# Performance work log

Hardware: AMD Instinct MI355X
Metric: run time of the kernel (lower is better)

The kernel has to match this reference:

```python
import jax, jax.numpy as jnp
import numpy as np

N = 50000
E = 800000
NODE_IN = 64
EDGE_IN = 8
OUT = 1
SAGE_DIMS = [(64, 64), (64, 64), (64, 32), (32, 32)]
EDGE_DIMS = [(8, 64), (64, 64), (64, 32), (32, 32)]


def setup_inputs():
    key = jax.random.key(0)
    keys = iter(jax.random.split(key, 64))
    d = {}
    d["x"] = jax.random.normal(next(keys), (N, NODE_IN), jnp.float32)
    d["dis"] = jax.random.normal(next(keys), (E, EDGE_IN), jnp.float32)
    d["edge_index"] = jax.random.randint(next(keys), (2, E), 0, N, dtype=jnp.int32)
    for i, (fi, fo) in enumerate(SAGE_DIMS):
        d[f"s{i}_wl"] = jax.random.normal(next(keys), (fi, fo), jnp.float32) / np.sqrt(fi).astype(np.float32)
        d[f"s{i}_bl"] = jnp.zeros((fo,), jnp.float32)
        d[f"s{i}_wr"] = jax.random.normal(next(keys), (fi, fo), jnp.float32) / np.sqrt(fi).astype(np.float32)
    for i, (fi, h) in enumerate(EDGE_DIMS):
        d[f"e{i}_w1"] = jax.random.normal(next(keys), (fi, 2 * h), jnp.float32) / np.sqrt(fi).astype(np.float32)
        d[f"e{i}_b1"] = jnp.zeros((2 * h,), jnp.float32)
        d[f"e{i}_w2"] = jax.random.normal(next(keys), (2 * h, h), jnp.float32) / np.sqrt(2 * h).astype(np.float32)
        d[f"e{i}_b2"] = jnp.zeros((h,), jnp.float32)
    d["fc_w"] = jax.random.normal(next(keys), (64, OUT), jnp.float32) / 8.0
    d["fc_b"] = jnp.zeros((OUT,), jnp.float32)
    return d


def _sage(x, row, col, wl, bl, wr):
    # PyG SAGEConv (aggr='mean'): lin_l(mean_{j->i} x_j) + lin_r(x_i); lin_l has bias.
    msg = x[row]  # [E, F] gather of source features
    s = jax.ops.segment_sum(msg, col, num_segments=N)
    cnt = jax.ops.segment_sum(jnp.ones((row.shape[0], 1), x.dtype), col, num_segments=N)
    mean = s / jnp.maximum(cnt, 1.0)  # isolated nodes -> 0 (matches scatter-mean)
    return mean @ wl + bl + x @ wr


def _edge_conv(dis, col, w1, b1, w2, b2):
    # EdgeOnlyConv: add_self_loops with num_nodes=E and zero edge_attr, so the
    # output has E rows; self-loop message = lin(0) = b1 and each segment t gets
    # mean = (sum_{edges->t} lin(dis) + b1) / (deg_in(t) + 1); then lin_update.
    msg = dis @ w1 + b1  # [E, 2h]
    s = jax.ops.segment_sum(msg, col, num_segments=E)
    deg = jax.ops.segment_sum(jnp.ones((col.shape[0], 1), dis.dtype), col, num_segments=E)
    aggr = (s + b1) / (deg + 1.0)
    return aggr @ w2 + b2


def _forward(x, dis, edge_index, sage_params, edge_params, fc_w, fc_b):
    row, col = edge_index[0], edge_index[1]
    h = x
    for wl, bl, wr in sage_params:
        h = jax.nn.leaky_relu(_sage(h, row, col, wl, bl, wr))
    d = dis
    for w1, b1, w2, b2 in edge_params:
        d = jax.nn.leaky_relu(_edge_conv(d, col, w1, b1, w2, b2))
    # dropout is identity at inference
    feats = jnp.concatenate([h[row] * h[col], d], axis=1)  # [E, hidden]
    return feats @ fc_w + fc_b


def reference(x, dis, edge_index, s0_wl, s0_bl, s0_wr, s1_wl, s1_bl, s1_wr, s2_wl, s2_bl, s2_wr, s3_wl, s3_bl, s3_wr, e0_w1, e0_b1, e0_w2, e0_b2, e1_w1, e1_b1, e1_w2, e1_b2, e2_w1, e2_b1, e2_w2, e2_b2, e3_w1, e3_b1, e3_w2, e3_b2, fc_w, fc_b):
    sage_params = [(s0_wl, s0_bl, s0_wr), (s1_wl, s1_bl, s1_wr), (s2_wl, s2_bl, s2_wr), (s3_wl, s3_bl, s3_wr)]
    edge_params = [(e0_w1, e0_b1, e0_w2, e0_b2), (e1_w1, e1_b1, e1_w2, e1_b2), (e2_w1, e2_b1, e2_w2, e2_b2), (e3_w1, e3_b1, e3_w2, e3_b2)]
    return _forward(x, dis, edge_index, sage_params, edge_params, fc_w, fc_b)
```

## Files before the change

kernel.cpp:

```cpp
#include <hip/hip_runtime.h>

#define LRELU(v) ((v) > 0.0f ? (v) : 0.01f * (v))

__device__ __forceinline__ unsigned short f2bf(float f) {
    union { float f; unsigned u; } c;
    c.f = f;
    return (unsigned short)((c.u + 0x7fffu + ((c.u >> 16) & 1)) >> 16);
}
__device__ __forceinline__ float bf_lo(unsigned u) {
    union { unsigned i; float f; } v;
    v.i = u << 16;
    return v.f;
}
__device__ __forceinline__ float bf_hi(unsigned u) {
    union { unsigned i; float f; } v;
    v.i = u & 0xffff0000u;
    return v.f;
}

__global__ void bucket_count_k(const int* __restrict__ col, int* __restrict__ bcnt, int E) {
    __shared__ int lcnt[512];
    int tid = threadIdx.x;
    for (int i = tid; i < 512; i += 1024) lcnt[i] = 0;
    __syncthreads();
    int base = blockIdx.x * 8192;
    for (int k = 0; k < 8; ++k) {
        int e = base + k * 1024 + tid;
        if (e < E) atomicAdd(&lcnt[col[e] >> 7], 1);
    }
    __syncthreads();
    for (int i = tid; i < 512; i += 1024) {
        int v = lcnt[i];
        if (v) atomicAdd(&bcnt[i], v);
    }
}

__global__ void bucket_scan_k(const int* __restrict__ bcnt, int* __restrict__ bbase,
                              int* __restrict__ bwp, int NBUCK, int E) {
    __shared__ int s[512];
    int tid = threadIdx.x;
    int v = (tid < NBUCK) ? bcnt[tid] : 0;
    s[tid] = v;
    __syncthreads();
    for (int off = 1; off < 512; off <<= 1) {
        int t = (tid >= off) ? s[tid - off] : 0;
        __syncthreads();
        s[tid] += t;
        __syncthreads();
    }
    if (tid < NBUCK) {
        int ex = s[tid] - v;
        bbase[tid] = ex;
        bwp[tid] = ex;
    }
    if (tid == 0) bbase[NBUCK] = E;
}

__global__ void bucket_scatter_k(const int* __restrict__ row, const int* __restrict__ col,
                                 int* __restrict__ bwp, int2* __restrict__ tmp, int E) {
    __shared__ int lcnt[512];
    __shared__ int gbase[512];
    int tid = threadIdx.x;
    for (int i = tid; i < 512; i += 1024) lcnt[i] = 0;
    __syncthreads();
    int base = blockIdx.x * 8192;
    int lpos[8], bk[8];
    for (int k = 0; k < 8; ++k) {
        int e = base + k * 1024 + tid;
        if (e < E) {
            int b = col[e] >> 7;
            bk[k] = b;
            lpos[k] = atomicAdd(&lcnt[b], 1);
        } else
            bk[k] = -1;
    }
    __syncthreads();
    for (int i = tid; i < 512; i += 1024) {
        int v = lcnt[i];
        gbase[i] = v ? atomicAdd(&bwp[i], v) : 0;
    }
    __syncthreads();
    for (int k = 0; k < 8; ++k) {
        int e = base + k * 1024 + tid;
        if (e < E) {
            int c = col[e];
            tmp[gbase[bk[k]] + lpos[k]] = make_int2(row[e], ((c & 127) << 25) | e);
        }
    }
}

__global__ void bucket_csr_k(const int2* __restrict__ tmp, const int* __restrict__ bbase,
                             int* __restrict__ rowptr, int* __restrict__ cnt,
                             int2* __restrict__ pairs, int N, int E) {
    constexpr int CAP = 6144;
    __shared__ int2 buf[CAP];
    __shared__ int lcnt[128];
    __shared__ int sscan[128];
    __shared__ int lwp[128];
    int b = blockIdx.x;
    int tid = threadIdx.x;
    int s = bbase[b], e = bbase[b + 1];
    int sz = e - s;
    if (tid < 128) lcnt[tid] = 0;
    __syncthreads();
    for (int i = tid; i < sz; i += 256) {
        int2 v = tmp[s + i];
        if (i < CAP) buf[i] = v;
        atomicAdd(&lcnt[((unsigned)v.y) >> 25], 1);
    }
    __syncthreads();
    if (tid < 128) sscan[tid] = lcnt[tid];
    __syncthreads();
    for (int off = 1; off < 128; off <<= 1) {
        int t = (tid < 128 && tid >= off) ? sscan[tid - off] : 0;
        __syncthreads();
        if (tid < 128) sscan[tid] += t;
        __syncthreads();
    }
    if (tid < 128) {
        int ex = sscan[tid] - lcnt[tid];
        lwp[tid] = ex;
        int c = b * 128 + tid;
        if (c < N) {
            rowptr[c] = s + ex;
            cnt[c] = lcnt[tid];
            if (c == N - 1) rowptr[N] = E;
        }
    }
    __syncthreads();
    for (int i = tid; i < sz; i += 256) {
        int2 v = (i < CAP) ? buf[i] : tmp[s + i];
        int cl = ((unsigned)v.y) >> 25;
        int p = atomicAdd(&lwp[cl], 1);
        pairs[s + p] = make_int2(v.x, v.y & 0x1FFFFFF);
    }
}

template <int FIN, int FOUT, bool BFL>
__global__ void gemm2_k(const float* __restrict__ h, const float* __restrict__ wl,
                        const float* __restrict__ wr, const float* __restrict__ bl,
                        void* __restrict__ hl, float* __restrict__ hr, int N) {
    constexpr int XT = (2 * FOUT) / 4;
    constexpr int YT = 256 / XT;
    constexpr int NPT = 4;
    constexpr int NPB = YT * NPT;
    __shared__ float sw[FIN * 2 * FOUT];
    int lin = threadIdx.y * XT + threadIdx.x;
    for (int idx = lin; idx < FIN * FOUT; idx += 256) {
        int f = idx / FOUT, o = idx % FOUT;
        sw[f * 2 * FOUT + o] = wl[idx];
        sw[f * 2 * FOUT + FOUT + o] = wr[idx];
    }
    __syncthreads();
    int og = threadIdx.x * 4;
    int base = blockIdx.x * NPB + threadIdx.y * NPT;
    int ix[NPT] = {min(base + 0, N - 1), min(base + 1, N - 1), min(base + 2, N - 1),
                   min(base + 3, N - 1)};
    float4 s[NPT] = {{0.f, 0.f, 0.f, 0.f}, {0.f, 0.f, 0.f, 0.f}, {0.f, 0.f, 0.f, 0.f},
                     {0.f, 0.f, 0.f, 0.f}};
#pragma unroll 2
    for (int f = 0; f < FIN; f += 4) {
        float4 w0 = *(const float4*)&sw[(f + 0) * 2 * FOUT + og];
        float4 w1 = *(const float4*)&sw[(f + 1) * 2 * FOUT + og];
        float4 w2 = *(const float4*)&sw[(f + 2) * 2 * FOUT + og];
        float4 w3 = *(const float4*)&sw[(f + 3) * 2 * FOUT + og];
#pragma unroll
        for (int k = 0; k < NPT; ++k) {
            float4 v = *(const float4*)(h + (size_t)ix[k] * FIN + f);
            s[k].x += v.x * w0.x + v.y * w1.x + v.z * w2.x + v.w * w3.x;
            s[k].y += v.x * w0.y + v.y * w1.y + v.z * w2.y + v.w * w3.y;
            s[k].z += v.x * w0.z + v.y * w1.z + v.z * w2.z + v.w * w3.z;
            s[k].w += v.x * w0.w + v.y * w1.w + v.z * w2.w + v.w * w3.w;
        }
    }
    bool isR = og >= FOUT;
    int oo = isR ? og - FOUT : og;
    if (isR) {
        float4 bias = *(const float4*)&bl[oo];
#pragma unroll
        for (int k = 0; k < NPT; ++k) {
            int i = base + k;
            if (i < N) {
                float4 r = {s[k].x + bias.x, s[k].y + bias.y, s[k].z + bias.z, s[k].w + bias.w};
                *(float4*)(hr + (size_t)i * FOUT + oo) = r;
            }
        }
    } else {
#pragma unroll
        for (int k = 0; k < NPT; ++k) {
            int i = base + k;
            if (i < N) {
                if (BFL) {
                    unsigned short* d = (unsigned short*)hl + (size_t)i * FOUT + oo;
                    *(ushort4*)d =
                        make_ushort4(f2bf(s[k].x), f2bf(s[k].y), f2bf(s[k].z), f2bf(s[k].w));
                } else {
                    *(float4*)((float*)hl + (size_t)i * FOUT + oo) = s[k];
                }
            }
        }
    }
}

__global__ void aggr_fused64_bf_k(const unsigned short* __restrict__ hlb,
                                  const float* __restrict__ hr, const int* __restrict__ rowptr,
                                  const int2* __restrict__ pairs, float* __restrict__ out, int N) {
    int wave = (blockIdx.x * blockDim.x + threadIdx.x) >> 6;
    int lane = threadIdx.x & 63;
    if (wave >= N) return;
    int u = lane >> 4, f4 = lane & 15;
    int s = rowptr[wave], e = rowptr[wave + 1];
    float4 a = {0.f, 0.f, 0.f, 0.f};
    int p = s + u;
    for (; p + 4 < e; p += 8) {
        int r0 = pairs[p].x, r1 = pairs[p + 4].x;
        uint2 v0 = ((const uint2*)(hlb + (size_t)r0 * 64))[f4];
        uint2 v1 = ((const uint2*)(hlb + (size_t)r1 * 64))[f4];
        a.x += bf_lo(v0.x) + bf_lo(v1.x);
        a.y += bf_hi(v0.x) + bf_hi(v1.x);
        a.z += bf_lo(v0.y) + bf_lo(v1.y);
        a.w += bf_hi(v0.y) + bf_hi(v1.y);
    }
    if (p < e) {
        uint2 v = ((const uint2*)(hlb + (size_t)pairs[p].x * 64))[f4];
        a.x += bf_lo(v.x); a.y += bf_hi(v.x); a.z += bf_lo(v.y); a.w += bf_hi(v.y);
    }
    a.x += __shfl_down(a.x, 32); a.y += __shfl_down(a.y, 32);
    a.z += __shfl_down(a.z, 32); a.w += __shfl_down(a.w, 32);
    a.x += __shfl_down(a.x, 16); a.y += __shfl_down(a.y, 16);
    a.z += __shfl_down(a.z, 16); a.w += __shfl_down(a.w, 16);
    if (lane < 16) {
        float inv = 1.0f / fmaxf((float)(e - s), 1.0f);
        float4 r = ((const float4*)(hr + (size_t)wave * 64))[f4];
        float4 o;
        o.x = LRELU(a.x * inv + r.x);
        o.y = LRELU(a.y * inv + r.y);
        o.z = LRELU(a.z * inv + r.z);
        o.w = LRELU(a.w * inv + r.w);
        ((float4*)(out + (size_t)wave * 64))[f4] = o;
    }
}

template <bool OUTBF>
__global__ void aggr_fused32_bf_k(const unsigned short* __restrict__ hlb,
                                  const float* __restrict__ hr, const int* __restrict__ rowptr,
                                  const int2* __restrict__ pairs, void* __restrict__ out, int N) {
    int wave = (blockIdx.x * blockDim.x + threadIdx.x) >> 6;
    int lane = threadIdx.x & 63;
    if (wave >= N) return;
    int u = lane >> 3, f4 = lane & 7;
    int s = rowptr[wave], e = rowptr[wave + 1];
    float4 a = {0.f, 0.f, 0.f, 0.f};
    int p = s + u;
    for (; p + 8 < e; p += 16) {
        int r0 = pairs[p].x, r1 = pairs[p + 8].x;
        uint2 v0 = ((const uint2*)(hlb + (size_t)r0 * 32))[f4];
        uint2 v1 = ((const uint2*)(hlb + (size_t)r1 * 32))[f4];
        a.x += bf_lo(v0.x) + bf_lo(v1.x);
        a.y += bf_hi(v0.x) + bf_hi(v1.x);
        a.z += bf_lo(v0.y) + bf_lo(v1.y);
        a.w += bf_hi(v0.y) + bf_hi(v1.y);
    }
    if (p < e) {
        uint2 v = ((const uint2*)(hlb + (size_t)pairs[p].x * 32))[f4];
        a.x += bf_lo(v.x); a.y += bf_hi(v.x); a.z += bf_lo(v.y); a.w += bf_hi(v.y);
    }
    a.x += __shfl_down(a.x, 32); a.y += __shfl_down(a.y, 32);
    a.z += __shfl_down(a.z, 32); a.w += __shfl_down(a.w, 32);
    a.x += __shfl_down(a.x, 16); a.y += __shfl_down(a.y, 16);
    a.z += __shfl_down(a.z, 16); a.w += __shfl_down(a.w, 16);
    a.x += __shfl_down(a.x, 8); a.y += __shfl_down(a.y, 8);
    a.z += __shfl_down(a.z, 8); a.w += __shfl_down(a.w, 8);
    if (lane < 8) {
        float inv = 1.0f / fmaxf((float)(e - s), 1.0f);
        const float4* hp = (const float4*)(hr + (size_t)wave * 32);
        float4 r = hp[f4];
        float4 o;
        o.x = LRELU(a.x * inv + r.x);
        o.y = LRELU(a.y * inv + r.y);
        o.z = LRELU(a.z * inv + r.z);
        o.w = LRELU(a.w * inv + r.w);
        if (OUTBF) {
            unsigned short* d = (unsigned short*)out + (size_t)wave * 32 + f4 * 4;
            *(ushort4*)d = make_ushort4(f2bf(o.x), f2bf(o.y), f2bf(o.z), f2bf(o.w));
        } else {
            ((float4*)((float*)out + (size_t)wave * 32))[f4] = o;
        }
    }
}

__global__ void edge_aggr8_k(const float* __restrict__ dis, const int* __restrict__ rowptr,
                             const int2* __restrict__ pairs, float* __restrict__ sd, int N) {
    int wave = (blockIdx.x * blockDim.x + threadIdx.x) >> 6;
    int lane = threadIdx.x & 63;
    if (wave >= N) return;
    int u = lane >> 1, f4 = lane & 1;
    int s = rowptr[wave], e = rowptr[wave + 1];
    float4 a = {0.f, 0.f, 0.f, 0.f};
    for (int p = s + u; p < e; p += 32) {
        const float4* dp = (const float4*)(dis + (size_t)pairs[p].y * 8);
        float4 v = dp[f4];
        a.x += v.x; a.y += v.y; a.z += v.z; a.w += v.w;
    }
    for (int off = 32; off >= 2; off >>= 1) {
        a.x += __shfl_down(a.x, off); a.y += __shfl_down(a.y, off);
        a.z += __shfl_down(a.z, off); a.w += __shfl_down(a.w, off);
    }
    if (lane < 2) ((float4*)(sd + (size_t)wave * 8))[f4] = a;
}

template <int H2, int HOUT>
__device__ __forceinline__ void w12_body(const float* __restrict__ w1,
                                         const float* __restrict__ w2, float* __restrict__ out,
                                         int i, int o) {
    float s = 0.0f;
#pragma unroll
    for (int k = 0; k < H2; ++k) s += w1[i * H2 + k] * w2[k * HOUT + o];
    out[i * HOUT + o] = s;
}

__global__ void gemm_w12_all_k(const float* __restrict__ w1_0, const float* __restrict__ w2_0,
                               float* __restrict__ o0, const float* __restrict__ w1_1,
                               const float* __restrict__ w2_1, float* __restrict__ o1,
                               const float* __restrict__ w1_2, const float* __restrict__ w2_2,
                               float* __restrict__ o2, const float* __restrict__ w1_3,
                               const float* __restrict__ w2_3, float* __restrict__ o3) {
    int b = blockIdx.x;
    int o = threadIdx.x;
    if (b < 8) {
        w12_body<128, 64>(w1_0, w2_0, o0, b, o);
    } else if (b < 72) {
        w12_body<128, 64>(w1_1, w2_1, o1, b - 8, o);
    } else if (b < 136) {
        if (o < 32) w12_body<64, 32>(w1_2, w2_2, o2, b - 72, o);
    } else {
        if (o < 32) w12_body<64, 32>(w1_3, w2_3, o3, b - 136, o);
    }
}

template <int FIN, int FOUT>
__global__ void edge_compute_scatter_k(const float* __restrict__ sd, const int* __restrict__ cnt,
                                       const float* __restrict__ w12, const float* __restrict__ mw2,
                                       const float* __restrict__ b1w2, const float* __restrict__ b2,
                                       const float* __restrict__ cnext,
                                       const int* __restrict__ col, float* __restrict__ sdnext,
                                       int N) {
    constexpr int ROWS = 256 / FOUT;
    constexpr int NPT = 4;
    constexpr int NPB = ROWS * NPT;
    __shared__ float sw[FIN * FOUT];
    int lin = threadIdx.y * FOUT + threadIdx.x;
    for (int idx = lin; idx < FIN * FOUT; idx += 256) sw[idx] = w12[idx];
    __syncthreads();
    int o = threadIdx.x;
    int base = blockIdx.x * NPB + threadIdx.y * NPT;
    int ix[NPT] = {min(base + 0, N - 1), min(base + 1, N - 1), min(base + 2, N - 1),
                   min(base + 3, N - 1)};
    float s[NPT] = {0.f, 0.f, 0.f, 0.f};
#pragma unroll 2
    for (int f = 0; f < FIN; f += 4) {
        float w0 = sw[(f + 0) * FOUT + o], w1 = sw[(f + 1) * FOUT + o];
        float w2 = sw[(f + 2) * FOUT + o], w3 = sw[(f + 3) * FOUT + o];
#pragma unroll
        for (int k = 0; k < NPT; ++k) {
            float4 v = *(const float4*)(sd + (size_t)ix[k] * FIN + f);
            s[k] += v.x * w0 + v.y * w1 + v.z * w2 + v.w * w3;
        }
    }
    float mo = mw2[o], bo = b1w2[o], b2o = b2[o], co = cnext[o];
#pragma unroll
    for (int k = 0; k < NPT; ++k) {
        int i = base + k;
        if (i < N) {
            float deg = (float)cnt[i];
            float inv = 1.0f / (deg + 1.0f);
            float val = LRELU((s[k] + deg * mo + bo) * inv + b2o);
            atomicAdd(&sdnext[(size_t)col[i] * FOUT + o], val - co);
        }
    }
}

template <int FIN, int FOUT>
__global__ void edge_compute2_k(const float* __restrict__ sd, const int* __restrict__ cnt,
                                const float* __restrict__ w12, const float* __restrict__ mw2,
                                const float* __restrict__ b1w2, const float* __restrict__ b2,
                                float* __restrict__ out, int N) {
    constexpr int ROWS = 256 / FOUT;
    constexpr int NPT = 4;
    constexpr int NPB = ROWS * NPT;
    __shared__ float sw[FIN * FOUT];
    int lin = threadIdx.y * FOUT + threadIdx.x;
    for (int idx = lin; idx < FIN * FOUT; idx += 256) sw[idx] = w12[idx];
    __syncthreads();
    int o = threadIdx.x;
    int base = blockIdx.x * NPB + threadIdx.y * NPT;
    int ix[NPT] = {min(base + 0, N - 1), min(base + 1, N - 1), min(base + 2, N - 1),
                   min(base + 3, N - 1)};
    float s[NPT] = {0.f, 0.f, 0.f, 0.f};
#pragma unroll 2
    for (int f = 0; f < FIN; f += 4) {
        float w0 = sw[(f + 0) * FOUT + o], w1 = sw[(f + 1) * FOUT + o];
        float w2 = sw[(f + 2) * FOUT + o], w3 = sw[(f + 3) * FOUT + o];
#pragma unroll
        for (int k = 0; k < NPT; ++k) {
            float4 v = *(const float4*)(sd + (size_t)ix[k] * FIN + f);
            s[k] += v.x * w0 + v.y * w1 + v.z * w2 + v.w * w3;
        }
    }
    float mo = mw2[o], bo = b1w2[o], b2o = b2[o];
#pragma unroll
    for (int k = 0; k < NPT; ++k) {
        int i = base + k;
        if (i < N) {
            float deg = (float)cnt[i];
            float inv = 1.0f / (deg + 1.0f);
            out[(size_t)i * FOUT + o] = LRELU((s[k] + deg * mo + bo) * inv + b2o);
        }
    }
}

__global__ void consts_k(const float* __restrict__ e0_b1, const float* __restrict__ e0_w2,
                         const float* __restrict__ e0_b2, const float* __restrict__ e1_b1,
                         const float* __restrict__ e1_w2, const float* __restrict__ e1_b2,
                         const float* __restrict__ e2_b1, const float* __restrict__ e2_w2,
                         const float* __restrict__ e2_b2, const float* __restrict__ e3_b1,
                         const float* __restrict__ e3_w2, const float* __restrict__ e3_b2,
                         const float* __restrict__ w12_1, const float* __restrict__ w12_2,
                         const float* __restrict__ w12_3, float* __restrict__ cbuf) {
    __shared__ float c1[64], c2[64], c3[32];
    int tid = threadIdx.x;
    if (tid < 64) {
        float s = 0.0f;
#pragma unroll
        for (int k = 0; k < 128; ++k) s += e0_b1[k] * e0_w2[k * 64 + tid];
        cbuf[192 + tid] = s;
        c1[tid] = LRELU(s + e0_b2[tid]);
        cbuf[tid] = c1[tid];
    }
    if (tid < 64) {
        float s = 0.0f;
#pragma unroll
        for (int k = 0; k < 128; ++k) s += e1_b1[k] * e1_w2[k * 64 + tid];
        cbuf[256 + tid] = s;
        c2[tid] = LRELU(s + e1_b2[tid]);
        cbuf[64 + tid] = c2[tid];
    }
    if (tid < 32) {
        float s = 0.0f;
#pragma unroll
        for (int k = 0; k < 64; ++k) s += e2_b1[k] * e2_w2[k * 32 + tid];
        cbuf[384 + tid] = s;
        c3[tid] = LRELU(s + e2_b2[tid]);
        cbuf[128 + tid] = c3[tid];
    }
    if (tid < 32) {
        float s = 0.0f;
#pragma unroll
        for (int k = 0; k < 64; ++k) s += e3_b1[k] * e3_w2[k * 32 + tid];
        cbuf[448 + tid] = s;
        cbuf[160 + tid] = LRELU(s + e3_b2[tid]);
    }
    __syncthreads();
    if (tid < 64) {
        float s = cbuf[256 + tid];
#pragma unroll
        for (int f = 0; f < 64; ++f) s += c1[f] * w12_1[f * 64 + tid];
        cbuf[320 + tid] = s;
    }
    if (tid < 32) {
        float s = cbuf[384 + tid];
#pragma unroll
        for (int f = 0; f < 64; ++f) s += c2[f] * w12_2[f * 32 + tid];
        cbuf[416 + tid] = s;
    }
    if (tid < 32) {
        float s = cbuf[448 + tid];
#pragma unroll
        for (int f = 0; f < 32; ++f) s += c3[f] * w12_3[f * 32 + tid];
        cbuf[480 + tid] = s;
    }
}

__device__ __forceinline__ float bdot8(uint4 a, uint4 b, const float* __restrict__ w) {
    return bf_lo(a.x) * bf_lo(b.x) * w[0] + bf_hi(a.x) * bf_hi(b.x) * w[1] +
           bf_lo(a.y) * bf_lo(b.y) * w[2] + bf_hi(a.y) * bf_hi(b.y) * w[3] +
           bf_lo(a.z) * bf_lo(b.z) * w[4] + bf_hi(a.z) * bf_hi(b.z) * w[5] +
           bf_lo(a.w) * bf_lo(b.w) * w[6] + bf_hi(a.w) * bf_hi(b.w) * w[7];
}

__global__ void final_k(const unsigned short* __restrict__ h3b, const float* __restrict__ dv3,
                        const float* __restrict__ c4, const int* __restrict__ row,
                        const int* __restrict__ col, const float* __restrict__ fcw,
                        const float* __restrict__ fcb, float* __restrict__ out, int E, int N) {
    __shared__ float sw[64];
    __shared__ float sc4[32];
    __shared__ float cdot_s;
    int tid = threadIdx.x;
    if (tid < 64) sw[tid] = fcw[tid];
    if (tid < 32) sc4[tid] = c4[tid];
    __syncthreads();
    if (tid == 0) {
        float cd = 0.0f;
#pragma unroll
        for (int k = 0; k < 32; ++k) cd += sc4[k] * sw[32 + k];
        cdot_s = cd;
    }
    __syncthreads();
    float fb = fcb[0];
    float cdot = cdot_s;
    int e0 = blockIdx.x * 512 + tid;
    int e1 = e0 + 256;
    bool v0 = e0 < E, v1 = e1 < E;
    int r0 = 0, c0 = 0, r1 = 0, c1 = 0;
    if (v0) { r0 = row[e0]; c0 = col[e0]; }
    if (v1) { r1 = row[e1]; c1 = col[e1]; }
    uint4 a00, a01, b00, b01, a10, a11, b10, b11;
    if (v0) {
        const uint4* pr = (const uint4*)(h3b + (size_t)r0 * 32);
        const uint4* pc = (const uint4*)(h3b + (size_t)c0 * 32);
        a00 = pr[0]; a01 = pr[1]; b00 = pc[0]; b01 = pc[1];
    }
    if (v1) {
        const uint4* pr = (const uint4*)(h3b + (size_t)r1 * 32);
        const uint4* pc = (const uint4*)(h3b + (size_t)c1 * 32);
        a10 = pr[0]; a11 = pr[1]; b10 = pc[0]; b11 = pc[1];
    }
    if (v0) {
        float s = fb + bdot8(a00, b00, sw) + bdot8(a01, b01, sw + 8) +
                  bdot8(((const uint4*)(h3b + (size_t)r0 * 32))[2],
                        ((const uint4*)(h3b + (size_t)c0 * 32))[2], sw + 16) +
                  bdot8(((const uint4*)(h3b + (size_t)r0 * 32))[3],
                        ((const uint4*)(h3b + (size_t)c0 * 32))[3], sw + 24);
        if (e0 < N) {
            const float4* dp = (const float4*)(dv3 + (size_t)e0 * 32);
#pragma unroll
            for (int q = 0; q < 8; ++q) {
                float4 d = dp[q];
                s += d.x * sw[32 + q * 4 + 0] + d.y * sw[32 + q * 4 + 1] +
                     d.z * sw[32 + q * 4 + 2] + d.w * sw[32 + q * 4 + 3];
            }
        } else {
            s += cdot;
        }
        out[e0] = s;
    }
    if (v1) {
        float s = fb + bdot8(a10, b10, sw) + bdot8(a11, b11, sw + 8) +
                  bdot8(((const uint4*)(h3b + (size_t)r1 * 32))[2],
                        ((const uint4*)(h3b + (size_t)c1 * 32))[2], sw + 16) +
                  bdot8(((const uint4*)(h3b + (size_t)r1 * 32))[3],
                        ((const uint4*)(h3b + (size_t)c1 * 32))[3], sw + 24);
        if (e1 < N) {
            const float4* dp = (const float4*)(dv3 + (size_t)e1 * 32);
#pragma unroll
            for (int q = 0; q < 8; ++q) {
                float4 d = dp[q];
                s += d.x * sw[32 + q * 4 + 0] + d.y * sw[32 + q * 4 + 1] +
                     d.z * sw[32 + q * 4 + 2] + d.w * sw[32 + q * 4 + 3];
            }
        } else {
            s += cdot;
        }
        out[e1] = s;
    }
}

extern "C" void kernel_launch(void* const* d_in, const int* in_sizes, int n_in, void* d_out,
                              int out_size, void* d_ws, size_t ws_size, hipStream_t stream) {
    const float* x = (const float*)d_in[0];
    const float* dis = (const float*)d_in[1];
    const int* ei = (const int*)d_in[2];
    const float* s_wl[4] = {(const float*)d_in[3], (const float*)d_in[6], (const float*)d_in[9],
                            (const float*)d_in[12]};
    const float* s_bl[4] = {(const float*)d_in[4], (const float*)d_in[7], (const float*)d_in[10],
                            (const float*)d_in[13]};
    const float* s_wr[4] = {(const float*)d_in[5], (const float*)d_in[8], (const float*)d_in[11],
                            (const float*)d_in[14]};
    const float* e_w1[4] = {(const float*)d_in[15], (const float*)d_in[19], (const float*)d_in[23],
                            (const float*)d_in[27]};
    const float* e_b1[4] = {(const float*)d_in[16], (const float*)d_in[20], (const float*)d_in[24],
                            (const float*)d_in[28]};
    const float* e_w2[4] = {(const float*)d_in[17], (const float*)d_in[21], (const float*)d_in[25],
                            (const float*)d_in[29]};
    const float* e_b2[4] = {(const float*)d_in[18], (const float*)d_in[22], (const float*)d_in[26],
                            (const float*)d_in[30]};
    const float* fcw = (const float*)d_in[31];
    const float* fcb = (const float*)d_in[32];

    const int N = in_sizes[0] / 64;
    const int E = in_sizes[1] / 8;
    const int* row = ei;
    const int* col = ei + E;
    const int NBUCK = (N + 127) / 128;
    const int EB = (E + 8191) / 8192;

    auto au = [](size_t v) { return (v + 255) & ~(size_t)255; };
    char* p = (char*)d_ws;
    int* cnt = (int*)p;       p += au((size_t)N * 4);
    int* rowptr = (int*)p;    p += au((size_t)(N + 1) * 4);
    int* bcnt = (int*)p;      p += au(512 * 4);
    int* bbase = (int*)p;     p += au(513 * 4);
    int* bwp = (int*)p;       p += au(512 * 4);
    float* w12_0 = (float*)p; p += au(512 * 4);
    float* w12_1 = (float*)p; p += au(4096 * 4);
    float* w12_2 = (float*)p; p += au(2048 * 4);
    float* w12_3 = (float*)p; p += au(1024 * 4);
    float* cbuf = (float*)p;  p += au(512 * 4);
    int2* pairs = (int2*)p;   p += au((size_t)E * 8);
    float* acc = (float*)p;   p += au((size_t)N * 64 * 4);
    float* hA = (float*)p;    p += au((size_t)N * 64 * 4);
    float* hB = (float*)p;    p += au((size_t)N * 64 * 4);
    float* dvA = (float*)p;   p += au((size_t)N * 64 * 4);
    float* dvB = (float*)p;   p += au((size_t)N * 64 * 4);

    int2* tmp = (int2*)dvA;
    unsigned short* hlb = (unsigned short*)acc;
    unsigned short* h3b = (unsigned short*)hA;

    hipMemsetAsync(bcnt, 0, 512 * 4, stream);
    bucket_count_k<<<EB, 1024, 0, stream>>>(col, bcnt, E);
    bucket_scan_k<<<1, 512, 0, stream>>>(bcnt, bbase, bwp, NBUCK, E);
    bucket_scatter_k<<<EB, 1024, 0, stream>>>(row, col, bwp, tmp, E);
    bucket_csr_k<<<NBUCK, 256, 0, stream>>>(tmp, bbase, rowptr, cnt, pairs, N, E);

    gemm_w12_all_k<<<168, 64, 0, stream>>>(e_w1[0], e_w2[0], w12_0, e_w1[1], e_w2[1], w12_1,
                                           e_w1[2], e_w2[2], w12_2, e_w1[3], e_w2[3], w12_3);
    consts_k<<<1, 128, 0, stream>>>(e_b1[0], e_w2[0], e_b2[0], e_b1[1], e_w2[1], e_b2[1], e_b1[2],
                                    e_w2[2], e_b2[2], e_b1[3], e_w2[3], e_b2[3], w12_1, w12_2,
                                    w12_3, cbuf);

    const int WPB = 4;

    gemm2_k<64, 64, true><<<(N + 31) / 32, dim3(32, 8), 0, stream>>>(x, s_wl[0], s_wr[0], s_bl[0],
                                                                     hlb, dvB, N);
    aggr_fused64_bf_k<<<(N + WPB - 1) / WPB, 256, 0, stream>>>(hlb, dvB, rowptr, pairs, hA, N);
    gemm2_k<64, 64, true><<<(N + 31) / 32, dim3(32, 8), 0, stream>>>(hA, s_wl[1], s_wr[1], s_bl[1],
                                                                     hlb, dvB, N);
    aggr_fused64_bf_k<<<(N + WPB - 1) / WPB, 256, 0, stream>>>(hlb, dvB, rowptr, pairs, hB, N);
    gemm2_k<64, 32, true><<<(N + 63) / 64, dim3(16, 16), 0, stream>>>(hB, s_wl[2], s_wr[2],
                                                                      s_bl[2], hlb, dvB, N);
    aggr_fused32_bf_k<false><<<(N + WPB - 1) / WPB, 256, 0, stream>>>(hlb, dvB, rowptr, pairs, hA,
                                                                      N);
    gemm2_k<32, 32, true><<<(N + 63) / 64, dim3(16, 16), 0, stream>>>(hA, s_wl[3], s_wr[3],
                                                                      s_bl[3], hlb, dvB, N);
    aggr_fused32_bf_k<true><<<(N + WPB - 1) / WPB, 256, 0, stream>>>(hlb, dvB, rowptr, pairs, h3b,
                                                                     N);

    edge_aggr8_k<<<(N + WPB - 1) / WPB, 256, 0, stream>>>(dis, rowptr, pairs, acc, N);
    hipMemsetAsync(dvA, 0, (size_t)N * 64 * 4, stream);
    edge_compute_scatter_k<8, 64><<<(N + 15) / 16, dim3(64, 4), 0, stream>>>(
        acc, cnt, w12_0, cbuf + 192, cbuf + 192, e_b2[0], cbuf + 0, col, dvA, N);
    hipMemsetAsync(acc, 0, (size_t)N * 64 * 4, stream);
    edge_compute_scatter_k<64, 64><<<(N + 15) / 16, dim3(64, 4), 0, stream>>>(
        dvA, cnt, w12_1, cbuf + 320, cbuf + 256, e_b2[1], cbuf + 64, col, acc, N);
    hipMemsetAsync(dvA, 0, (size_t)N * 32 * 4, stream);
    edge_compute_scatter_k<64, 32><<<(N + 31) / 32, dim3(32, 8), 0, stream>>>(
        acc, cnt, w12_2, cbuf + 416, cbuf + 384, e_b2[2], cbuf + 128, col, dvA, N);
    edge_compute2_k<32, 32><<<(N + 31) / 32, dim3(32, 8), 0, stream>>>(
        dvA, cnt, w12_3, cbuf + 480, cbuf + 448, e_b2[3], dvB, N);

    final_k<<<(E + 511) / 512, 256, 0, stream>>>(h3b, dvB, cbuf + 160, row, col, fcw, fcb,
                                                 (float*)d_out, E, N);
}
```

Baseline: 482.7 us.

## Split CSR pairs, fold memsets into kernels, merge constant kernels, precompute edge dot

Splits the interleaved (row, edge-id) pair array into two separate int arrays so each gather kernel reads only the field it needs. Removes the hipMemsetAsync calls by zeroing the next scatter buffer inside the preceding kernels, and merges the weight-product and bias-constant kernels plus the bucket-count reset into one launch. The last edge layer now reduces its output against the fc weights per node, so the final kernel reads one float instead of 32. This trades several launches and some bandwidth for extra work inside the existing kernels and a more intricate buffer-reuse scheme.

New measurement: 467.2 us. 1.03x faster.

```diff
diff --git a/kernel.cpp b/kernel.cpp
--- a/kernel.cpp
+++ b/kernel.cpp
@@ -91,7 +91,7 @@
 
 __global__ void bucket_csr_k(const int2* __restrict__ tmp, const int* __restrict__ bbase,
                              int* __restrict__ rowptr, int* __restrict__ cnt,
-                             int2* __restrict__ pairs, int N, int E) {
+                             int* __restrict__ rows, int* __restrict__ eids, int N, int E) {
     constexpr int CAP = 6144;
     __shared__ int2 buf[CAP];
     __shared__ int lcnt[128];
@@ -132,7 +132,8 @@
         int2 v = (i < CAP) ? buf[i] : tmp[s + i];
         int cl = ((unsigned)v.y) >> 25;
         int p = atomicAdd(&lwp[cl], 1);
-        pairs[s + p] = make_int2(v.x, v.y & 0x1FFFFFF);
+        rows[s + p] = v.x;
+        eids[s + p] = v.y & 0x1FFFFFF;
     }
 }
 
@@ -204,7 +205,7 @@
 
 __global__ void aggr_fused64_bf_k(const unsigned short* __restrict__ hlb,
                                   const float* __restrict__ hr, const int* __restrict__ rowptr,
-                                  const int2* __restrict__ pairs, float* __restrict__ out, int N) {
+                                  const int* __restrict__ rows, float* __restrict__ out, int N) {
     int wave = (blockIdx.x * blockDim.x + threadIdx.x) >> 6;
     int lane = threadIdx.x & 63;
     if (wave >= N) return;
@@ -213,7 +214,7 @@
     float4 a = {0.f, 0.f, 0.f, 0.f};
     int p = s + u;
     for (; p + 4 < e; p += 8) {
-        int r0 = pairs[p].x, r1 = pairs[p + 4].x;
+        int r0 = rows[p], r1 = rows[p + 4];
         uint2 v0 = ((const uint2*)(hlb + (size_t)r0 * 64))[f4];
         uint2 v1 = ((const uint2*)(hlb + (size_t)r1 * 64))[f4];
         a.x += bf_lo(v0.x) + bf_lo(v1.x);
@@ -222,7 +223,7 @@
         a.w += bf_hi(v0.y) + bf_hi(v1.y);
     }
     if (p < e) {
-        uint2 v = ((const uint2*)(hlb + (size_t)pairs[p].x * 64))[f4];
+        uint2 v = ((const uint2*)(hlb + (size_t)rows[p] * 64))[f4];
         a.x += bf_lo(v.x); a.y += bf_hi(v.x); a.z += bf_lo(v.y); a.w += bf_hi(v.y);
     }
     a.x += __shfl_down(a.x, 32); a.y += __shfl_down(a.y, 32);
@@ -244,7 +245,7 @@
 template <bool OUTBF>
 __global__ void aggr_fused32_bf_k(const unsigned short* __restrict__ hlb,
                                   const float* __restrict__ hr, const int* __restrict__ rowptr,
-                                  const int2* __restrict__ pairs, void* __restrict__ out, int N) {
+                                  const int* __restrict__ rows, void* __restrict__ out, int N) {
     int wave = (blockIdx.x * blockDim.x + threadIdx.x) >> 6;
     int lane = threadIdx.x & 63;
     if (wave >= N) return;
@@ -253,7 +254,7 @@
     float4 a = {0.f, 0.f, 0.f, 0.f};
     int p = s + u;
     for (; p + 8 < e; p += 16) {
-        int r0 = pairs[p].x, r1 = pairs[p + 8].x;
+        int r0 = rows[p], r1 = rows[p + 8];
         uint2 v0 = ((const uint2*)(hlb + (size_t)r0 * 32))[f4];
         uint2 v1 = ((const uint2*)(hlb + (size_t)r1 * 32))[f4];
         a.x += bf_lo(v0.x) + bf_lo(v1.x);
@@ -262,7 +263,7 @@
         a.w += bf_hi(v0.y) + bf_hi(v1.y);
     }
     if (p < e) {
-        uint2 v = ((const uint2*)(hlb + (size_t)pairs[p].x * 32))[f4];
+        uint2 v = ((const uint2*)(hlb + (size_t)rows[p] * 32))[f4];
         a.x += bf_lo(v.x); a.y += bf_hi(v.x); a.z += bf_lo(v.y); a.w += bf_hi(v.y);
     }
     a.x += __shfl_down(a.x, 32); a.y += __shfl_down(a.y, 32);
@@ -290,15 +291,17 @@
 }
 
 __global__ void edge_aggr8_k(const float* __restrict__ dis, const int* __restrict__ rowptr,
-                             const int2* __restrict__ pairs, float* __restrict__ sd, int N) {
+                             const int* __restrict__ eids, float* __restrict__ sd,
+                             float* __restrict__ zbuf, int N) {
     int wave = (blockIdx.x * blockDim.x + threadIdx.x) >> 6;
     int lane = threadIdx.x & 63;
     if (wave >= N) return;
+    zbuf[(size_t)wave * 64 + lane] = 0.0f;
     int u = lane >> 1, f4 = lane & 1;
     int s = rowptr[wave], e = rowptr[wave + 1];
     float4 a = {0.f, 0.f, 0.f, 0.f};
     for (int p = s + u; p < e; p += 32) {
-        const float4* dp = (const float4*)(dis + (size_t)pairs[p].y * 8);
+        const float4* dp = (const float4*)(dis + (size_t)eids[p] * 8);
         float4 v = dp[f4];
         a.x += v.x; a.y += v.y; a.z += v.z; a.w += v.w;
     }
@@ -319,22 +322,93 @@
     out[i * HOUT + o] = s;
 }
 
-__global__ void gemm_w12_all_k(const float* __restrict__ w1_0, const float* __restrict__ w2_0,
-                               float* __restrict__ o0, const float* __restrict__ w1_1,
-                               const float* __restrict__ w2_1, float* __restrict__ o1,
-                               const float* __restrict__ w1_2, const float* __restrict__ w2_2,
-                               float* __restrict__ o2, const float* __restrict__ w1_3,
-                               const float* __restrict__ w2_3, float* __restrict__ o3) {
+__global__ void w12c_k(const float* __restrict__ w1_0, const float* __restrict__ w2_0,
+                       float* __restrict__ o0, const float* __restrict__ w1_1,
+                       const float* __restrict__ w2_1, float* __restrict__ o1,
+                       const float* __restrict__ w1_2, const float* __restrict__ w2_2,
+                       float* __restrict__ o2, const float* __restrict__ w1_3,
+                       const float* __restrict__ w2_3, float* __restrict__ o3,
+                       const float* __restrict__ b1_0, const float* __restrict__ b2_0,
+                       const float* __restrict__ b1_1, const float* __restrict__ b2_1,
+                       const float* __restrict__ b1_2, const float* __restrict__ b2_2,
+                       const float* __restrict__ b1_3, const float* __restrict__ b2_3,
+                       float* cbuf, int* __restrict__ bcnt) {
     int b = blockIdx.x;
     int o = threadIdx.x;
     if (b < 8) {
-        w12_body<128, 64>(w1_0, w2_0, o0, b, o);
+        if (o < 64) w12_body<128, 64>(w1_0, w2_0, o0, b, o);
     } else if (b < 72) {
-        w12_body<128, 64>(w1_1, w2_1, o1, b - 8, o);
+        if (o < 64) w12_body<128, 64>(w1_1, w2_1, o1, b - 8, o);
     } else if (b < 136) {
         if (o < 32) w12_body<64, 32>(w1_2, w2_2, o2, b - 72, o);
+    } else if (b < 168) {
+        if (o < 32) w12_body<64, 32>(w1_3, w2_3, o3, b - 136, o);
+    } else if (b == 168) {
+        __shared__ float c1[64], c2[64], c3[32], u1[128], u2[64], u3[64];
+        float t;
+        if (o < 64) {
+            t = 0.0f;
+#pragma unroll
+            for (int k = 0; k < 128; ++k) t += b1_0[k] * w2_0[k * 64 + o];
+            cbuf[192 + o] = t;
+            c1[o] = LRELU(t + b2_0[o]);
+            cbuf[o] = c1[o];
+            t = 0.0f;
+#pragma unroll
+            for (int k = 0; k < 128; ++k) t += b1_1[k] * w2_1[k * 64 + o];
+            cbuf[256 + o] = t;
+            c2[o] = LRELU(t + b2_1[o]);
+            cbuf[64 + o] = c2[o];
+        }
+        if (o < 32) {
+            t = 0.0f;
+#pragma unroll
+            for (int k = 0; k < 64; ++k) t += b1_2[k] * w2_2[k * 32 + o];
+            cbuf[384 + o] = t;
+            c3[o] = LRELU(t + b2_2[o]);
+            cbuf[128 + o] = c3[o];
+            t = 0.0f;
+#pragma unroll
+            for (int k = 0; k < 64; ++k) t += b1_3[k] * w2_3[k * 32 + o];
+            cbuf[448 + o] = t;
+            cbuf[160 + o] = LRELU(t + b2_3[o]);
+        }
+        __syncthreads();
+        {
+            float s = 0.0f;
+#pragma unroll
+            for (int f = 0; f < 64; ++f) s += c1[f] * w1_1[f * 128 + o];
+            u1[o] = s;
+        }
+        if (o < 64) {
+            float s = 0.0f;
+#pragma unroll
+            for (int f = 0; f < 64; ++f) s += c2[f] * w1_2[f * 64 + o];
+            u2[o] = s;
+            float s3 = 0.0f;
+#pragma unroll
+            for (int f = 0; f < 32; ++f) s3 += c3[f] * w1_3[f * 64 + o];
+            u3[o] = s3;
+        }
+        __syncthreads();
+        if (o < 64) {
+            float s = cbuf[256 + o];
+#pragma unroll
+            for (int k = 0; k < 128; ++k) s += u1[k] * w2_1[k * 64 + o];
+            cbuf[320 + o] = s;
+        }
+        if (o < 32) {
+            float s = cbuf[384 + o];
+#pragma unroll
+            for (int k = 0; k < 64; ++k) s += u2[k] * w2_2[k * 32 + o];
+            cbuf[416 + o] = s;
+            float s3 = cbuf[448 + o];
+#pragma unroll
+            for (int k = 0; k < 64; ++k) s3 += u3[k] * w2_3[k * 32 + o];
+            cbuf[480 + o] = s3;
+        }
     } else {
-        if (o < 32) w12_body<64, 32>(w1_3, w2_3, o3, b - 136, o);
+        bcnt[o] = 0; bcnt[o + 128] = 0; bcnt[o + 256] = 0; bcnt[o + 384] = 0;
     }
 }
 
@@ -344,7 +418,7 @@
                                        const float* __restrict__ b1w2, const float* __restrict__ b2,
                                        const float* __restrict__ cnext,
                                        const int* __restrict__ col, float* __restrict__ sdnext,
-                                       int N) {
+                                       int N, float* __restrict__ zbuf, int zf4) {
     constexpr int ROWS = 256 / FOUT;
     constexpr int NPT = 4;
     constexpr int NPB = ROWS * NPT;
@@ -352,6 +426,11 @@
     int lin = threadIdx.y * FOUT + threadIdx.x;
     for (int idx = lin; idx < FIN * FOUT; idx += 256) sw[idx] = w12[idx];
     __syncthreads();
+    if (zf4) {
+        float4 z4 = {0.f, 0.f, 0.f, 0.f};
+        for (int z = blockIdx.x * 256 + lin; z < zf4; z += gridDim.x * 256)
+            ((float4*)zbuf)[z] = z4;
+    }
     int o = threadIdx.x;
     int base = blockIdx.x * NPB + threadIdx.y * NPT;
     int ix[NPT] = {min(base + 0, N - 1), min(base + 1, N - 1), min(base + 2, N - 1),
@@ -380,14 +459,13 @@
     }
 }
 
-template <int FIN, int FOUT>
-__global__ void edge_compute2_k(const float* __restrict__ sd, const int* __restrict__ cnt,
-                                const float* __restrict__ w12, const float* __restrict__ mw2,
-                                const float* __restrict__ b1w2, const float* __restrict__ b2,
-                                float* __restrict__ out, int N) {
-    constexpr int ROWS = 256 / FOUT;
+__global__ void edge_dot_k(const float* __restrict__ sd, const int* __restrict__ cnt,
+                           const float* __restrict__ w12, const float* __restrict__ mw2,
+                           const float* __restrict__ b1w2, const float* __restrict__ b2,
+                           const float* __restrict__ fcw, float* __restrict__ ddot, int N) {
+    constexpr int FIN = 32, FOUT = 32;
     constexpr int NPT = 4;
-    constexpr int NPB = ROWS * NPT;
+    constexpr int NPB = (256 / FOUT) * NPT;
     __shared__ float sw[FIN * FOUT];
     int lin = threadIdx.y * FOUT + threadIdx.x;
     for (int idx = lin; idx < FIN * FOUT; idx += 256) sw[idx] = w12[idx];
@@ -407,77 +485,18 @@
             s[k] += v.x * w0 + v.y * w1 + v.z * w2 + v.w * w3;
         }
     }
-    float mo = mw2[o], bo = b1w2[o], b2o = b2[o];
+    float mo = mw2[o], bo = b1w2[o], b2o = b2[o], fw = fcw[32 + o];
 #pragma unroll
     for (int k = 0; k < NPT; ++k) {
-        int i = base + k;
-        if (i < N) {
-            float deg = (float)cnt[i];
-            float inv = 1.0f / (deg + 1.0f);
-            out[(size_t)i * FOUT + o] = LRELU((s[k] + deg * mo + bo) * inv + b2o);
-        }
-    }
-}
-
-__global__ void consts_k(const float* __restrict__ e0_b1, const float* __restrict__ e0_w2,
-                         const float* __restrict__ e0_b2, const float* __restrict__ e1_b1,
-                         const float* __restrict__ e1_w2, const float* __restrict__ e1_b2,
-                         const float* __restrict__ e2_b1, const float* __restrict__ e2_w2,
-                         const float* __restrict__ e2_b2, const float* __restrict__ e3_b1,
-                         const float* __restrict__ e3_w2, const float* __restrict__ e3_b2,
-                         const float* __restrict__ w12_1, const float* __restrict__ w12_2,
-                         const float* __restrict__ w12_3, float* __restrict__ cbuf) {
-    __shared__ float c1[64], c2[64], c3[32];
-    int tid = threadIdx.x;
-    if (tid < 64) {
-        float s = 0.0f;
-#pragma unroll
-        for (int k = 0; k < 128; ++k) s += e0_b1[k] * e0_w2[k * 64 + tid];
-        cbuf[192 + tid] = s;
-        c1[tid] = LRELU(s + e0_b2[tid]);
-        cbuf[tid] = c1[tid];
-    }
-    if (tid < 64) {
-        float s = 0.0f;
-#pragma unroll
-        for (int k = 0; k < 128; ++k) s += e1_b1[k] * e1_w2[k * 64 + tid];
-        cbuf[256 + tid] = s;
-        c2[tid] = LRELU(s + e1_b2[tid]);
-        cbuf[64 + tid] = c2[tid];
-    }
-    if (tid < 32) {
-        float s = 0.0f;
-#pragma unroll
-        for (int k = 0; k < 64; ++k) s += e2_b1[k] * e2_w2[k * 32 + tid];
-        cbuf[384 + tid] = s;
-        c3[tid] = LRELU(s + e2_b2[tid]);
-        cbuf[128 + tid] = c3[tid];
-    }
-    if (tid < 32) {
-        float s = 0.0f;
-#pragma unroll
-        for (int k = 0; k < 64; ++k) s += e3_b1[k] * e3_w2[k * 32 + tid];
-        cbuf[448 + tid] = s;
-        cbuf[160 + tid] = LRELU(s + e3_b2[tid]);
-    }
-    __syncthreads();
-    if (tid < 64) {
-        float s = cbuf[256 + tid];
-#pragma unroll
-        for (int f = 0; f < 64; ++f) s += c1[f] * w12_1[f * 64 + tid];
-        cbuf[320 + tid] = s;
-    }
-    if (tid < 32) {
-        float s = cbuf[384 + tid];
-#pragma unroll
-        for (int f = 0; f < 64; ++f) s += c2[f] * w12_2[f * 32 + tid];
-        cbuf[416 + tid] = s;
-    }
-    if (tid < 32) {
-        float s = cbuf[448 + tid];
-#pragma unroll
-        for (int f = 0; f < 32; ++f) s += c3[f] * w12_3[f * 32 + tid];
-        cbuf[480 + tid] = s;
+        float deg = (float)cnt[ix[k]];
+        float inv = 1.0f / (deg + 1.0f);
+        float v = LRELU((s[k] + deg * mo + bo) * inv + b2o) * fw;
+        v += __shfl_down(v, 16);
+        v += __shfl_down(v, 8);
+        v += __shfl_down(v, 4);
+        v += __shfl_down(v, 2);
+        v += __shfl_down(v, 1);
+        if (o == 0 && base + k < N) ddot[base + k] = v;
     }
 }
 
@@ -488,7 +507,7 @@
            bf_lo(a.w) * bf_lo(b.w) * w[6] + bf_hi(a.w) * bf_hi(b.w) * w[7];
 }
 
-__global__ void final_k(const unsigned short* __restrict__ h3b, const float* __restrict__ dv3,
+__global__ void final_k(const unsigned short* __restrict__ h3b, const float* __restrict__ ddot,
                         const float* __restrict__ c4, const int* __restrict__ row,
                         const int* __restrict__ col, const float* __restrict__ fcw,
                         const float* __restrict__ fcb, float* __restrict__ out, int E, int N) {
@@ -531,17 +550,7 @@
                         ((const uint4*)(h3b + (size_t)c0 * 32))[2], sw + 16) +
                   bdot8(((const uint4*)(h3b + (size_t)r0 * 32))[3],
                         ((const uint4*)(h3b + (size_t)c0 * 32))[3], sw + 24);
-        if (e0 < N) {
-            const float4* dp = (const float4*)(dv3 + (size_t)e0 * 32);
-#pragma unroll
-            for (int q = 0; q < 8; ++q) {
-                float4 d = dp[q];
-                s += d.x * sw[32 + q * 4 + 0] + d.y * sw[32 + q * 4 + 1] +
-                     d.z * sw[32 + q * 4 + 2] + d.w * sw[32 + q * 4 + 3];
-            }
-        } else {
-            s += cdot;
-        }
+        s += (e0 < N) ? ddot[e0] : cdot;
         out[e0] = s;
     }
     if (v1) {
@@ -550,17 +559,7 @@
                         ((const uint4*)(h3b + (size_t)c1 * 32))[2], sw + 16) +
                   bdot8(((const uint4*)(h3b + (size_t)r1 * 32))[3],
                         ((const uint4*)(h3b + (size_t)c1 * 32))[3], sw + 24);
-        if (e1 < N) {
-            const float4* dp = (const float4*)(dv3 + (size_t)e1 * 32);
-#pragma unroll
-            for (int q = 0; q < 8; ++q) {
-                float4 d = dp[q];
-                s += d.x * sw[32 + q * 4 + 0] + d.y * sw[32 + q * 4 + 1] +
-                     d.z * sw[32 + q * 4 + 2] + d.w * sw[32 + q * 4 + 3];
-            }
-        } else {
-            s += cdot;
-        }
+        s += (e1 < N) ? ddot[e1] : cdot;
         out[e1] = s;
     }
 }
@@ -606,7 +605,8 @@
     float* w12_2 = (float*)p; p += au(2048 * 4);
     float* w12_3 = (float*)p; p += au(1024 * 4);
     float* cbuf = (float*)p;  p += au(512 * 4);
-    int2* pairs = (int2*)p;   p += au((size_t)E * 8);
+    int* rowsA = (int*)p;     p += au((size_t)E * 4);
+    int* eidsA = (int*)p;     p += au((size_t)E * 4);
     float* acc = (float*)p;   p += au((size_t)N * 64 * 4);
     float* hA = (float*)p;    p += au((size_t)N * 64 * 4);
     float* hB = (float*)p;    p += au((size_t)N * 64 * 4);
@@ -616,49 +616,45 @@
     int2* tmp = (int2*)dvA;
     unsigned short* hlb = (unsigned short*)acc;
     unsigned short* h3b = (unsigned short*)hA;
-
-    hipMemsetAsync(bcnt, 0, 512 * 4, stream);
+    float* ddot = dvB;
+
+    w12c_k<<<170, 128, 0, stream>>>(e_w1[0], e_w2[0], w12_0, e_w1[1], e_w2[1], w12_1, e_w1[2],
+                                    e_w2[2], w12_2, e_w1[3], e_w2[3], w12_3, e_b1[0], e_b2[0],
+                                    e_b1[1], e_b2[1], e_b1[2], e_b2[2], e_b1[3], e_b2[3], cbuf,
+                                    bcnt);
+
     bucket_count_k<<<EB, 1024, 0, stream>>>(col, bcnt, E);
     bucket_scan_k<<<1, 512, 0, stream>>>(bcnt, bbase, bwp, NBUCK, E);
     bucket_scatter_k<<<EB, 1024, 0, stream>>>(row, col, bwp, tmp, E);
-    bucket_csr_k<<<NBUCK, 256, 0, stream>>>(tmp, bbase, rowptr, cnt, pairs, N, E);
-
-    gemm_w12_all_k<<<168, 64, 0, stream>>>(e_w1[0], e_w2[0], w12_0, e_w1[1], e_w2[1], w12_1,
-                                           e_w1[2], e_w2[2], w12_2, e_w1[3], e_w2[3], w12_3);
-    consts_k<<<1, 128, 0, stream>>>(e_b1[0], e_w2[0], e_b2[0], e_b1[1], e_w2[1], e_b2[1], e_b1[2],
-                                    e_w2[2], e_b2[2], e_b1[3], e_w2[3], e_b2[3], w12_1, w12_2,
-                                    w12_3, cbuf);
+    bucket_csr_k<<<NBUCK, 256, 0, stream>>>(tmp, bbase, rowptr, cnt, rowsA, eidsA, N, E);
 
     const int WPB = 4;
 
     gemm2_k<64, 64, true><<<(N + 31) / 32, dim3(32, 8), 0, stream>>>(x, s_wl[0], s_wr[0], s_bl[0],
                                                                      hlb, dvB, N);
-    aggr_fused64_bf_k<<<(N + WPB - 1) / WPB, 256, 0, stream>>>(hlb, dvB, rowptr, pairs, hA, N);
+    aggr_fused64_bf_k<<<(N + WPB - 1) / WPB, 256, 0, stream>>>(hlb, dvB, rowptr, rowsA, hA, N);
     gemm2_k<64, 64, true><<<(N + 31) / 32, dim3(32, 8), 0, stream>>>(hA, s_wl[1], s_wr[1], s_bl[1],
                                                                      hlb, dvB, N);
-    aggr_fused64_bf_k<<<(N + WPB - 1) / WPB, 256, 0, stream>>>(hlb, dvB, rowptr, pairs, hB, N);
+    aggr_fused64_bf_k<<<(N + WPB - 1) / WPB, 256, 0, stream>>>(hlb, dvB, rowptr, rowsA, hB, N);
     gemm2_k<64, 32, true><<<(N + 63) / 64, dim3(16, 16), 0, stream>>>(hB, s_wl[2], s_wr[2],
                                                                       s_bl[2], hlb, dvB, N);
-    aggr_fused32_bf_k<false><<<(N + WPB - 1) / WPB, 256, 0, stream>>>(hlb, dvB, rowptr, pairs, hA,
+    aggr_fused32_bf_k<false><<<(N + WPB - 1) / WPB, 256, 0, stream>>>(hlb, dvB, rowptr, rowsA, hA,
                                                                       N);
     gemm2_k<32, 32, true><<<(N + 63) / 64, dim3(16, 16), 0, stream>>>(hA, s_wl[3], s_wr[3],
                                                                       s_bl[3], hlb, dvB, N);
-    aggr_fused32_bf_k<true><<<(N + WPB - 1) / WPB, 256, 0, stream>>>(hlb, dvB, rowptr, pairs, h3b,
+    aggr_fused32_bf_k<true><<<(N + WPB - 1) / WPB, 256, 0, stream>>>(hlb, dvB, rowptr, rowsA, h3b,
                                                                      N);
 
-    edge_aggr8_k<<<(N + WPB - 1) / WPB, 256, 0, stream>>>(dis, rowptr, pairs, acc, N);
-    hipMemsetAsync(dvA, 0, (size_t)N * 64 * 4, stream);
+    edge_aggr8_k<<<(N + WPB - 1) / WPB, 256, 0, stream>>>(dis, rowptr, eidsA, hB, dvA, N);
     edge_compute_scatter_k<8, 64><<<(N + 15) / 16, dim3(64, 4), 0, stream>>>(
-        acc, cnt, w12_0, cbuf + 192, cbuf + 192, e_b2[0], cbuf + 0, col, dvA, N);
-    hipMemsetAsync(acc, 0, (size_t)N * 64 * 4, stream);
+        hB, cnt, w12_0, cbuf + 192, cbuf + 192, e_b2[0], cbuf + 0, col, dvA, N, acc, N * 16);
     edge_compute_scatter_k<64, 64><<<(N + 15) / 16, dim3(64, 4), 0, stream>>>(
-        dvA, cnt, w12_1, cbuf + 320, cbuf + 256, e_b2[1], cbuf + 64, col, acc, N);
-    hipMemsetAsync(dvA, 0, (size_t)N * 32 * 4, stream);
+        dvA, cnt, w12_1, cbuf + 320, cbuf + 256, e_b2[1], cbuf + 64, col, acc, N, hB, N * 8);
     edge_compute_scatter_k<64, 32><<<(N + 31) / 32, dim3(32, 8), 0, stream>>>(
-        acc, cnt, w12_2, cbuf + 416, cbuf + 384, e_b2[2], cbuf + 128, col, dvA, N);
-    edge_compute2_k<32, 32><<<(N + 31) / 32, dim3(32, 8), 0, stream>>>(
-        dvA, cnt, w12_3, cbuf + 480, cbuf + 448, e_b2[3], dvB, N);
-
-    final_k<<<(E + 511) / 512, 256, 0, stream>>>(h3b, dvB, cbuf + 160, row, col, fcw, fcb,
+        acc, cnt, w12_2, cbuf + 416, cbuf + 384, e_b2[2], cbuf + 128, col, hB, N, nullptr, 0);
+    edge_dot_k<<<(N + 31) / 32, dim3(32, 8), 0, stream>>>(hB, cnt, w12_3, cbuf + 480, cbuf + 448,
+                                                          e_b2[3], fcw, ddot, N);
+
+    final_k<<<(E + 511) / 512, 256, 0, stream>>>(h3b, ddot, cbuf + 160, row, col, fcw, fcb,
                                                  (float*)d_out, E, N);
 }
```
